# Optimization experiments

Hardware: AMD Instinct MI355X
Metric: run time of the kernel (lower is better)

The kernel has to match this reference:

```python
import jax, jax.numpy as jnp
import numpy as np

N = 20000      # nodes
E = 320000     # edges (before self loops)
F_IN = 256     # num_node_features
H = 8          # heads
C = 64         # dim_h per head
B = 64         # graphs in batch
NC = 10        # num_classes
HID = H * C    # 512


def setup_inputs() -> dict:
    key = jax.random.key(0)
    ks = jax.random.split(key, 20)
    def glorot(k, shape, fan):
        return jax.random.normal(k, shape, jnp.float32) / np.sqrt(fan)
    inp = {
        'x': jax.random.normal(ks[0], (N, F_IN), jnp.float32),
        'edge_index': jax.random.randint(ks[1], (2, E), 0, N),
        'batch': jnp.sort(jax.random.randint(ks[2], (N,), 0, B)),
        # conv1: F_IN -> H*C
        'W1': glorot(ks[3], (F_IN, HID), F_IN),
        'a_src1': glorot(ks[4], (H, C), C),
        'a_dst1': glorot(ks[5], (H, C), C),
        'b1': jnp.zeros((HID,), jnp.float32),
        # conv2: HID -> H*C
        'W2': glorot(ks[6], (HID, HID), HID),
        'a_src2': glorot(ks[7], (H, C), C),
        'a_dst2': glorot(ks[8], (H, C), C),
        'b2': jnp.zeros((HID,), jnp.float32),
        # conv3: HID -> H*C
        'W3': glorot(ks[9], (HID, HID), HID),
        'a_src3': glorot(ks[10], (H, C), C),
        'a_dst3': glorot(ks[11], (H, C), C),
        'b3': jnp.zeros((HID,), jnp.float32),
        # final classifier
        'Wl': glorot(ks[12], (HID, NC), HID),
        'bl': jnp.zeros((NC,), jnp.float32),
    }
    return inp


def _gat_conv(x, src, dst, W, a_src, a_dst, b):
    """PyG GATConv (concat=True, negative_slope=0.2). src/dst include self loops."""
    xt = (x @ W).reshape(-1, H, C)                      # [N, H, C]
    al_s = jnp.einsum('nhc,hc->nh', xt, a_src)          # [N, H]
    al_d = jnp.einsum('nhc,hc->nh', xt, a_dst)
    e = jax.nn.leaky_relu(al_s[src] + al_d[dst], 0.2)   # [E', H]
    m = jax.ops.segment_max(e, dst, num_segments=N)     # segment softmax (stable)
    m = jax.lax.stop_gradient(jnp.where(jnp.isfinite(m), m, 0.0))
    p = jnp.exp(e - m[dst])
    s = jax.ops.segment_sum(p, dst, num_segments=N)
    alpha = p / (s[dst] + 1e-16)                        # [E', H]
    msg = xt[src] * alpha[..., None]                    # [E', H, C]
    out = jax.ops.segment_sum(msg, dst, num_segments=N) # [N, H, C]
    return out.reshape(-1, HID) + b


def reference(x, edge_index, batch, W1, a_src1, a_dst1, b1,
              W2, a_src2, a_dst2, b2, W3, a_src3, a_dst3, b3, Wl, bl):
    loop = jnp.arange(N, dtype=edge_index.dtype)
    src = jnp.concatenate([edge_index[0], loop])        # add_self_loops=True
    dst = jnp.concatenate([edge_index[1], loop])

    h = jax.nn.elu(_gat_conv(x, src, dst, W1, a_src1, a_dst1, b1))
    h = jax.nn.elu(_gat_conv(h, src, dst, W2, a_src2, a_dst2, b2))
    h = jax.nn.elu(_gat_conv(h, src, dst, W3, a_src3, a_dst3, b3))

    # global mean pool over graphs
    cnt = jax.ops.segment_sum(jnp.ones((N,), h.dtype), batch, num_segments=B)
    hG = jax.ops.segment_sum(h, batch, num_segments=B) / jnp.clip(cnt, 1.0)[:, None]

    # dropout p=0.5 is identity in eval mode
    logits = hG @ Wl + bl
    return hG, jax.nn.softmax(logits, axis=1)
```

## Files before the change

kernel.cpp:

```cpp
#include <hip/hip_runtime.h>
#include <hip/hip_bf16.h>
#include <math.h>

#define N_NODES  20000
#define E_EDGES  320000
#define E_TOT    (E_EDGES + N_NODES)
#define F_INF    256
#define HEADS    8
#define CDIM     64
#define HID      512
#define B_GRAPHS 64
#define NCLS     10
#define M_PAD    20096
#define NSCAN    20
#define NWG_GEMM 1256

typedef __attribute__((ext_vector_type(8))) short short8;
typedef __attribute__((ext_vector_type(4))) float f32x4;

__device__ inline unsigned short f2bf(float x) {
    unsigned u = __builtin_bit_cast(unsigned, x);
    u += 0x7fff + ((u >> 16) & 1);
    return (unsigned short)(u >> 16);
}
__device__ inline float bf2f(unsigned short h) {
    unsigned u = ((unsigned)h) << 16;
    return __builtin_bit_cast(float, u);
}

#define GLOAD_LDS16(g, l) __builtin_amdgcn_global_load_lds(                     \
        (const __attribute__((address_space(1))) void*)(g),                     \
        (__attribute__((address_space(3))) void*)(l), 16, 0, 0)

__global__ __launch_bounds__(256) void split_pad(const float* __restrict__ src,
                                                 unsigned short* __restrict__ hi,
                                                 unsigned short* __restrict__ lo,
                                                 int M, int K, long total) {
    long i = ((long)blockIdx.x * 256 + threadIdx.x) * 4;
    if (i >= total) return;
    int row = (int)(i / K);
    float4 v = make_float4(0.f, 0.f, 0.f, 0.f);
    if (row < M) v = *(const float4*)(src + i);
    ushort4 h, l;
    h.x = f2bf(v.x); l.x = f2bf(v.x - bf2f(h.x));
    h.y = f2bf(v.y); l.y = f2bf(v.y - bf2f(h.y));
    h.z = f2bf(v.z); l.z = f2bf(v.z - bf2f(h.z));
    h.w = f2bf(v.w); l.w = f2bf(v.w - bf2f(h.w));
    *(ushort4*)(hi + i) = h;
    *(ushort4*)(lo + i) = l;
}

__global__ __launch_bounds__(256) void transpose_split_B(const float* __restrict__ B,
                                                         unsigned short* __restrict__ Bthi,
                                                         unsigned short* __restrict__ Btlo,
                                                         int K) {
    __shared__ float t[32][33];
    int n0 = blockIdx.x * 32, k0 = blockIdx.y * 32;
    int tx = threadIdx.x & 31, ty = threadIdx.x >> 5;
    for (int i = ty; i < 32; i += 8) t[i][tx] = B[(size_t)(k0 + i) * HID + n0 + tx];
    __syncthreads();
    for (int i = ty; i < 32; i += 8) {
        float v = t[tx][i];
        unsigned short h = f2bf(v);
        unsigned short l = f2bf(v - bf2f(h));
        Bthi[(size_t)(n0 + i) * K + k0 + tx] = h;
        Btlo[(size_t)(n0 + i) * K + k0 + tx] = l;
    }
}

__global__ __launch_bounds__(256) void gemm_mfma(const unsigned short* __restrict__ Ahi,
                                                 const unsigned short* __restrict__ Alo,
                                                 const unsigned short* __restrict__ Bhi,
                                                 const unsigned short* __restrict__ Blo,
                                                 const float* __restrict__ a_src,
                                                 const float* __restrict__ a_dst,
                                                 unsigned short* __restrict__ xtb,
                                                 float* __restrict__ al_s,
                                                 float* __restrict__ al_d,
                                                 int M, int K) {
    __shared__ short AsHi[4096], AsLo[4096], BsHi[2048], BsLo[2048];
    const int tid = threadIdx.x;
    const int w = tid >> 6, lane = tid & 63;

    const int xcd = blockIdx.x & 7, idx = blockIdx.x >> 3;
    const int wg = xcd * (NWG_GEMM >> 3) + idx;
    const int row0 = (wg >> 3) * 128, col0 = (wg & 7) * 64;

    long offA[2];
    int ldsA[2];
#pragma unroll
    for (int i = 0; i < 2; ++i) {
        int u = w * 128 + i * 64 + lane;
        int row = u >> 2;
        int kg = (u & 3) ^ ((row >> 1) & 3);
        offA[i] = ((long)(row0 + row) * K + kg * 8) * 2;
        ldsA[i] = (w * 128 + i * 64) * 8;
    }
    long offB;
    int ldsB;
    {
        int u = w * 64 + lane;
        int row = u >> 2;
        int kg = (u & 3) ^ ((row >> 1) & 3);
        offB = ((long)(col0 + row) * K + kg * 8) * 2;
        ldsB = (w * 64) * 8;
    }

    const int r16 = lane & 15, kg = lane >> 4;
    int aOff[2], bOff[4];
#pragma unroll
    for (int i = 0; i < 2; ++i) {
        int row = w * 32 + i * 16 + r16;
        aOff[i] = (row * 4 + (kg ^ ((row >> 1) & 3))) * 16;
    }
#pragma unroll
    for (int j = 0; j < 4; ++j) {
        int col = j * 16 + r16;
        bOff[j] = (col * 4 + (kg ^ ((col >> 1) & 3))) * 16;
    }

    const char* pAhi = (const char*)Ahi;
    const char* pAlo = (const char*)Alo;
    const char* pBhi = (const char*)Bhi;
    const char* pBlo = (const char*)Blo;

    f32x4 acc[2][4] = {};

    for (int kk = 0; kk < K; kk += 32) {
        long kb = (long)kk * 2;
        __syncthreads();
#pragma unroll
        for (int i = 0; i < 2; ++i) {
            GLOAD_LDS16(pAhi + offA[i] + kb, AsHi + ldsA[i]);
            GLOAD_LDS16(pAlo + offA[i] + kb, AsLo + ldsA[i]);
        }
        GLOAD_LDS16(pBhi + offB + kb, BsHi + ldsB);
        GLOAD_LDS16(pBlo + offB + kb, BsLo + ldsB);
        __syncthreads();

        short8 fah[2], fal[2], fbh[4], fbl[4];
#pragma unroll
        for (int i = 0; i < 2; ++i) {
            fah[i] = *(const short8*)((const char*)AsHi + aOff[i]);
            fal[i] = *(const short8*)((const char*)AsLo + aOff[i]);
        }
#pragma unroll
        for (int j = 0; j < 4; ++j) {
            fbh[j] = *(const short8*)((const char*)BsHi + bOff[j]);
            fbl[j] = *(const short8*)((const char*)BsLo + bOff[j]);
        }
#pragma unroll
        for (int i = 0; i < 2; ++i)
#pragma unroll
            for (int j = 0; j < 4; ++j) {
                acc[i][j] = __builtin_amdgcn_mfma_f32_16x16x32_bf16(fah[i], fbh[j], acc[i][j], 0, 0, 0);
                acc[i][j] = __builtin_amdgcn_mfma_f32_16x16x32_bf16(fah[i], fbl[j], acc[i][j], 0, 0, 0);
                acc[i][j] = __builtin_amdgcn_mfma_f32_16x16x32_bf16(fal[i], fbh[j], acc[i][j], 0, 0, 0);
            }
    }

    const int h = col0 >> 6;
    float asv[4], adv[4];
#pragma unroll
    for (int j = 0; j < 4; ++j) {
        asv[j] = a_src[h * CDIM + j * 16 + r16];
        adv[j] = a_dst[h * CDIM + j * 16 + r16];
    }
#pragma unroll
    for (int i = 0; i < 2; ++i) {
        int rbase = row0 + w * 32 + i * 16 + (lane >> 4) * 4;
#pragma unroll
        for (int rr = 0; rr < 4; ++rr) {
            float ss = acc[i][0][rr] * asv[0] + acc[i][1][rr] * asv[1]
                     + acc[i][2][rr] * asv[2] + acc[i][3][rr] * asv[3];
            float dd = acc[i][0][rr] * adv[0] + acc[i][1][rr] * adv[1]
                     + acc[i][2][rr] * adv[2] + acc[i][3][rr] * adv[3];
#pragma unroll
            for (int off = 1; off < 16; off <<= 1) {
                ss += __shfl_xor(ss, off);
                dd += __shfl_xor(dd, off);
            }
            int row = rbase + rr;
            if ((lane & 15) == 0 && row < M) {
                al_s[row * HEADS + h] = ss;
                al_d[row * HEADS + h] = dd;
            }
        }
#pragma unroll
        for (int j = 0; j < 4; ++j) {
            int col = col0 + j * 16 + r16;
#pragma unroll
            for (int rr = 0; rr < 4; ++rr)
                if (rbase + rr < M) xtb[(size_t)(rbase + rr) * HID + col] = f2bf(acc[i][j][rr]);
        }
    }
}

__global__ __launch_bounds__(256) void count_edges(const int* __restrict__ ei,
                                                   int* __restrict__ counts) {
    int e = blockIdx.x * 256 + threadIdx.x;
    if (e < E_TOT) {
        int dst = (e < E_EDGES) ? ei[E_EDGES + e] : (e - E_EDGES);
        atomicAdd(&counts[dst], 1);
    }
}

__global__ __launch_bounds__(1024) void scan_local(const int* __restrict__ counts,
                                                   int* __restrict__ incl,
                                                   int* __restrict__ bsum,
                                                   const int* __restrict__ batch,
                                                   int* __restrict__ bounds) {
    __shared__ int s[1024];
    int tid = threadIdx.x;
    int i = blockIdx.x * 1024 + tid;
    if (blockIdx.x == 0 && tid <= B_GRAPHS) {
        int lo = 0, hi = N_NODES;
        while (lo < hi) {
            int mid = (lo + hi) >> 1;
            if (batch[mid] < tid) lo = mid + 1; else hi = mid;
        }
        bounds[tid] = lo;
    }
    int v = (i < N_NODES) ? counts[i] : 0;
    s[tid] = v;
    __syncthreads();
    for (int off = 1; off < 1024; off <<= 1) {
        int t = (tid >= off) ? s[tid - off] : 0;
        __syncthreads();
        s[tid] += t;
        __syncthreads();
    }
    if (i < N_NODES) incl[i] = s[tid];
    if (tid == 1023) bsum[blockIdx.x] = s[1023];
}

__global__ __launch_bounds__(1024) void scan_finalize(const int* __restrict__ counts,
                                                      const int* __restrict__ incl,
                                                      const int* __restrict__ bsum,
                                                      int* __restrict__ offsets,
                                                      int* __restrict__ cursor) {
    __shared__ int bpre_s;
    if (threadIdx.x == 0) {
        int s = 0;
        for (int j = 0; j < blockIdx.x; ++j) s += bsum[j];
        bpre_s = s;
    }
    __syncthreads();
    int i = blockIdx.x * 1024 + threadIdx.x;
    if (i < N_NODES) {
        int inc = incl[i] + bpre_s;
        offsets[i + 1] = inc;
        cursor[i] = inc - counts[i];
    }
    if (i == 0) offsets[0] = 0;
}

__global__ __launch_bounds__(256) void scatter_edges(const int* __restrict__ ei,
                                                     int* __restrict__ cursor,
                                                     int* __restrict__ csr) {
    int e = blockIdx.x * 256 + threadIdx.x;
    if (e < E_TOT) {
        int srcn, dst;
        if (e < E_EDGES) { srcn = ei[e]; dst = ei[E_EDGES + e]; }
        else             { srcn = dst = e - E_EDGES; }
        int pos = atomicAdd(&cursor[dst], 1);
        csr[pos] = srcn;
    }
}

__global__ __launch_bounds__(256) void gat_aggregate4(const unsigned short* __restrict__ xtb,
                                                      const float* __restrict__ al_s,
                                                      const float* __restrict__ al_d,
                                                      const int* __restrict__ offsets,
                                                      const int* __restrict__ csr,
                                                      const float* __restrict__ bias,
                                                      unsigned short* __restrict__ outHi,
                                                      unsigned short* __restrict__ outLo) {
    const int lane = threadIdx.x & 63;
    const int n = blockIdx.x * 4 + (threadIdx.x >> 6);
    const int h = lane >> 3;
    const int c0 = lane * 8;
    const int beg = offsets[n];
    const int deg = offsets[n + 1] - beg;
    const float aldv = al_d[n * HEADS + h];

    float acc[8] = {};
    float psum = 0.f;

#pragma unroll 4
    for (int i = 0; i < deg; ++i) {
        int srcn = csr[beg + i];
        float ev = al_s[srcn * HEADS + h] + aldv;
        ev = (ev >= 0.f) ? ev : 0.2f * ev;
        float p = __expf(ev);
        psum += p;
        short8 row = *(const short8*)(xtb + (size_t)srcn * HID + c0);
#pragma unroll
        for (int j = 0; j < 8; ++j)
            acc[j] = fmaf(p, bf2f((unsigned short)row[j]), acc[j]);
    }

    const float inv = 1.f / (psum + 1e-16f);
    float4 b0 = *(const float4*)(bias + c0);
    float4 b1 = *(const float4*)(bias + c0 + 4);
    float bv[8] = { b0.x, b0.y, b0.z, b0.w, b1.x, b1.y, b1.z, b1.w };
    short8 h8, l8;
#pragma unroll
    for (int j = 0; j < 8; ++j) {
        float v = acc[j] * inv + bv[j];
        v = (v > 0.f) ? v : expm1f(v);
        unsigned short hi = f2bf(v);
        h8[j] = (short)hi;
        l8[j] = (short)f2bf(v - bf2f(hi));
    }
    size_t o = (size_t)n * HID + c0;
    *(short8*)(outHi + o) = h8;
    *(short8*)(outLo + o) = l8;
}

__global__ __launch_bounds__(256) void pool_partial(const unsigned short* __restrict__ hHi,
                                                    const unsigned short* __restrict__ hLo,
                                                    const int* __restrict__ bounds,
                                                    float* __restrict__ partial) {
    const int b = blockIdx.x, y = blockIdx.y, k = blockIdx.z;
    const int s = bounds[b], cnt = bounds[b + 1] - s;
    const int ns = s + (cnt * k) / 4;
    const int ne = s + (cnt * (k + 1)) / 4;
    const int t = threadIdx.x;
    const int chp = t & 31;
    const int nl = t >> 5;

    float a0 = 0.f, a1 = 0.f;
    for (int n = ns + nl; n < ne; n += 8) {
        size_t off = (size_t)n * HID + y * 64 + chp * 2;
        unsigned vh = *(const unsigned*)(hHi + off);
        unsigned vl = *(const unsigned*)(hLo + off);
        a0 += bf2f((unsigned short)(vh & 0xffff)) + bf2f((unsigned short)(vl & 0xffff));
        a1 += bf2f((unsigned short)(vh >> 16)) + bf2f((unsigned short)(vl >> 16));
    }
    __shared__ float red[4][32][2];
    a0 += __shfl_xor(a0, 32);
    a1 += __shfl_xor(a1, 32);
    if ((t & 63) < 32) { red[t >> 6][chp][0] = a0; red[t >> 6][chp][1] = a1; }
    __syncthreads();
    if (t < 64) {
        int cp = t >> 1, c = t & 1;
        float v = red[0][cp][c] + red[1][cp][c] + red[2][cp][c] + red[3][cp][c];
        partial[(((size_t)k * B_GRAPHS + b) * 8 + y) * 64 + cp * 2 + c] = v;
    }
}

__global__ __launch_bounds__(512) void pool_classify(const float* __restrict__ partial,
                                                     const int* __restrict__ bounds,
                                                     const float* __restrict__ Wl,
                                                     const float* __restrict__ bl,
                                                     float* __restrict__ hG,
                                                     float* __restrict__ outP) {
    const int b = blockIdx.x, t = threadIdx.x;
    __shared__ float row[HID];
    __shared__ float logit[NCLS];
    float v = 0.f;
#pragma unroll
    for (int k = 0; k < 4; ++k)
        v += partial[((size_t)k * B_GRAPHS + b) * HID + t];
    float cnt = fmaxf((float)(bounds[b + 1] - bounds[b]), 1.0f);
    v /= cnt;
    hG[b * HID + t] = v;
    row[t] = v;
    __syncthreads();
    if (t < NCLS) {
        float acc = bl[t];
        for (int j = 0; j < HID; ++j) acc += row[j] * Wl[j * NCLS + t];
        logit[t] = acc;
    }
    __syncthreads();
    if (t == 0) {
        float mx = logit[0];
        for (int k = 1; k < NCLS; ++k) mx = fmaxf(mx, logit[k]);
        float ssum = 0.f, ex[NCLS];
        for (int k = 0; k < NCLS; ++k) { ex[k] = expf(logit[k] - mx); ssum += ex[k]; }
        for (int k = 0; k < NCLS; ++k) outP[b * NCLS + k] = ex[k] / ssum;
    }
}

extern "C" void kernel_launch(void* const* d_in, const int* in_sizes, int n_in,
                              void* d_out, int out_size, void* d_ws, size_t ws_size,
                              hipStream_t stream) {
    const float* x     = (const float*)d_in[0];
    const int*   ei    = (const int*)d_in[1];
    const int*   batch = (const int*)d_in[2];
    const float* W[3]  = { (const float*)d_in[3], (const float*)d_in[7],  (const float*)d_in[11] };
    const float* as_[3] = { (const float*)d_in[4], (const float*)d_in[8],  (const float*)d_in[12] };
    const float* ad_[3] = { (const float*)d_in[5], (const float*)d_in[9],  (const float*)d_in[13] };
    const float* bb[3] = { (const float*)d_in[6], (const float*)d_in[10], (const float*)d_in[14] };
    const float* Wl    = (const float*)d_in[15];
    const float* bl    = (const float*)d_in[16];

    char* ws = (char*)d_ws;
    unsigned short* A1hi = (unsigned short*)ws;      ws += (size_t)M_PAD * F_INF * 2;
    unsigned short* A1lo = (unsigned short*)ws;      ws += (size_t)M_PAD * F_INF * 2;
    unsigned short* A2hi = (unsigned short*)ws;      ws += (size_t)M_PAD * HID * 2;
    unsigned short* A2lo = (unsigned short*)ws;      ws += (size_t)M_PAD * HID * 2;
    unsigned short* Bthi = (unsigned short*)ws;      ws += (size_t)HID * HID * 2;
    unsigned short* Btlo = (unsigned short*)ws;      ws += (size_t)HID * HID * 2;
    unsigned short* xtb  = (unsigned short*)ws;      ws += (size_t)N_NODES * HID * 2;
    float* als  = (float*)ws;                        ws += (size_t)N_NODES * HEADS * 4;
    float* ald  = (float*)ws;                        ws += (size_t)N_NODES * HEADS * 4;
    float* partial = (float*)ws;                     ws += (size_t)4 * B_GRAPHS * HID * 4;
    int* counts  = (int*)ws;                         ws += (size_t)N_NODES * 4;
    int* incl    = (int*)ws;                         ws += (size_t)N_NODES * 4;
    int* bsum    = (int*)ws;                         ws += 32 * 4;
    int* offsets = (int*)ws;                         ws += (size_t)(N_NODES + 1) * 4;
    int* cursor  = (int*)ws;                         ws += (size_t)N_NODES * 4;
    int* csr     = (int*)ws;                         ws += (size_t)E_TOT * 4;
    int* bounds  = (int*)ws;                         ws += (size_t)(B_GRAPHS + 1) * 4;

    float* hG = (float*)d_out;
    float* probs = (float*)d_out + (size_t)B_GRAPHS * HID;

    hipMemsetAsync(counts, 0, (size_t)N_NODES * 4, stream);
    count_edges<<<(E_TOT + 255) / 256, 256, 0, stream>>>(ei, counts);
    scan_local<<<NSCAN, 1024, 0, stream>>>(counts, incl, bsum, batch, bounds);
    scan_finalize<<<NSCAN, 1024, 0, stream>>>(counts, incl, bsum, offsets, cursor);
    scatter_edges<<<(E_TOT + 255) / 256, 256, 0, stream>>>(ei, cursor, csr);
    hipMemsetAsync(A2hi + (size_t)N_NODES * HID, 0, (size_t)(M_PAD - N_NODES) * HID * 2, stream);
    hipMemsetAsync(A2lo + (size_t)N_NODES * HID, 0, (size_t)(M_PAD - N_NODES) * HID * 2, stream);

    {
        long totA = (long)M_PAD * F_INF;
        split_pad<<<(int)(totA / 4 / 256), 256, 0, stream>>>(x, A1hi, A1lo, N_NODES, F_INF, totA);
        transpose_split_B<<<dim3(HID / 32, F_INF / 32), 256, 0, stream>>>(W[0], Bthi, Btlo, F_INF);
        gemm_mfma<<<NWG_GEMM, 256, 0, stream>>>(A1hi, A1lo, Bthi, Btlo, as_[0], ad_[0],
                                                xtb, als, ald, N_NODES, F_INF);
        gat_aggregate4<<<N_NODES / 4, 256, 0, stream>>>(xtb, als, ald, offsets, csr, bb[0], A2hi, A2lo);
    }

    for (int L = 1; L < 3; ++L) {
        transpose_split_B<<<dim3(HID / 32, HID / 32), 256, 0, stream>>>(W[L], Bthi, Btlo, HID);
        gemm_mfma<<<NWG_GEMM, 256, 0, stream>>>(A2hi, A2lo, Bthi, Btlo, as_[L], ad_[L],
                                                xtb, als, ald, N_NODES, HID);
        gat_aggregate4<<<N_NODES / 4, 256, 0, stream>>>(xtb, als, ald, offsets, csr, bb[L], A2hi, A2lo);
    }

    {
        dim3 pgrid(B_GRAPHS, 8, 4);
        pool_partial<<<pgrid, 256, 0, stream>>>(A2hi, A2lo, bounds, partial);
        pool_classify<<<B_GRAPHS, 512, 0, stream>>>(partial, bounds, Wl, bl, hG, probs);
    }
}
```

Measured before the change: 379.4 us.

## Double-buffer GEMM LDS tiles and batch all weight transposes into one launch

The GEMM main loop now uses two LDS buffers, issuing the async global-to-LDS loads for the next K-slice before computing the current one, with explicit vmcnt waits and raw barriers in place of two __syncthreads per iteration. The three per-layer weight transpose/split kernels are merged into a single 3D-grid launch at the start, writing into separate per-layer buffers. This aims to hide global-load latency behind MFMA work and remove two kernel launches. The cost is doubled LDS use per workgroup, which may reduce occupancy, plus extra workspace for the weight copies.

```diff
diff --git a/kernel.cpp b/kernel.cpp
--- a/kernel.cpp
+++ b/kernel.cpp
@@ -50,10 +50,22 @@
     *(ushort4*)(lo + i) = l;
 }
 
-__global__ __launch_bounds__(256) void transpose_split_B(const float* __restrict__ B,
-                                                         unsigned short* __restrict__ Bthi,
-                                                         unsigned short* __restrict__ Btlo,
-                                                         int K) {
+__global__ __launch_bounds__(256) void transpose_split_all(const float* __restrict__ W1,
+                                                           const float* __restrict__ W2,
+                                                           const float* __restrict__ W3,
+                                                           unsigned short* __restrict__ B1h,
+                                                           unsigned short* __restrict__ B1l,
+                                                           unsigned short* __restrict__ B2h,
+                                                           unsigned short* __restrict__ B2l,
+                                                           unsigned short* __restrict__ B3h,
+                                                           unsigned short* __restrict__ B3l) {
+    const int L = blockIdx.z;
+    const int K = (L == 0) ? F_INF : HID;
+    if (blockIdx.y * 32 >= K) return;
+    const float* B = (L == 0) ? W1 : (L == 1) ? W2 : W3;
+    unsigned short* Bh = (L == 0) ? B1h : (L == 1) ? B2h : B3h;
+    unsigned short* Bl = (L == 0) ? B1l : (L == 1) ? B2l : B3l;
+
     __shared__ float t[32][33];
     int n0 = blockIdx.x * 32, k0 = blockIdx.y * 32;
     int tx = threadIdx.x & 31, ty = threadIdx.x >> 5;
@@ -63,8 +75,8 @@
         float v = t[tx][i];
         unsigned short h = f2bf(v);
         unsigned short l = f2bf(v - bf2f(h));
-        Bthi[(size_t)(n0 + i) * K + k0 + tx] = h;
-        Btlo[(size_t)(n0 + i) * K + k0 + tx] = l;
+        Bh[(size_t)(n0 + i) * K + k0 + tx] = h;
+        Bl[(size_t)(n0 + i) * K + k0 + tx] = l;
     }
 }
 
@@ -78,7 +90,7 @@
                                                  float* __restrict__ al_s,
                                                  float* __restrict__ al_d,
                                                  int M, int K) {
-    __shared__ short AsHi[4096], AsLo[4096], BsHi[2048], BsLo[2048];
+    __shared__ short AsHi[2][4096], AsLo[2][4096], BsHi[2][2048], BsLo[2][2048];
     const int tid = threadIdx.x;
     const int w = tid >> 6, lane = tid & 63;
 
@@ -126,38 +138,57 @@
 
     f32x4 acc[2][4] = {};
 
-    for (int kk = 0; kk < K; kk += 32) {
-        long kb = (long)kk * 2;
-        __syncthreads();
-#pragma unroll
-        for (int i = 0; i < 2; ++i) {
-            GLOAD_LDS16(pAhi + offA[i] + kb, AsHi + ldsA[i]);
-            GLOAD_LDS16(pAlo + offA[i] + kb, AsLo + ldsA[i]);
+#define STAGE(buf, kk) do {                                                      \
+        long kb = (long)(kk) * 64;                                               \
+        _Pragma("unroll")                                                        \
+        for (int i_ = 0; i_ < 2; ++i_) {                                         \
+            GLOAD_LDS16(pAhi + offA[i_] + kb, &AsHi[buf][ldsA[i_]]);             \
+            GLOAD_LDS16(pAlo + offA[i_] + kb, &AsLo[buf][ldsA[i_]]);             \
+        }                                                                        \
+        GLOAD_LDS16(pBhi + offB + kb, &BsHi[buf][ldsB]);                         \
+        GLOAD_LDS16(pBlo + offB + kb, &BsLo[buf][ldsB]);                         \
+    } while (0)
+
+#define COMPUTE(buf) do {                                                        \
+        short8 fah[2], fal[2], fbh[4], fbl[4];                                   \
+        _Pragma("unroll")                                                        \
+        for (int i_ = 0; i_ < 2; ++i_) {                                         \
+            fah[i_] = *(const short8*)((const char*)AsHi[buf] + aOff[i_]);       \
+            fal[i_] = *(const short8*)((const char*)AsLo[buf] + aOff[i_]);       \
+        }                                                                        \
+        _Pragma("unroll")                                                        \
+        for (int j_ = 0; j_ < 4; ++j_) {                                         \
+            fbh[j_] = *(const short8*)((const char*)BsHi[buf] + bOff[j_]);       \
+            fbl[j_] = *(const short8*)((const char*)BsLo[buf] + bOff[j_]);       \
+        }                                                                        \
+        _Pragma("unroll")                                                        \
+        for (int i_ = 0; i_ < 2; ++i_)                                           \
+            _Pragma("unroll")                                                    \
+            for (int j_ = 0; j_ < 4; ++j_) {                                     \
+                acc[i_][j_] = __builtin_amdgcn_mfma_f32_16x16x32_bf16(fah[i_], fbh[j_], acc[i_][j_], 0, 0, 0); \
+                acc[i_][j_] = __builtin_amdgcn_mfma_f32_16x16x32_bf16(fah[i_], fbl[j_], acc[i_][j_], 0, 0, 0); \
+                acc[i_][j_] = __builtin_amdgcn_mfma_f32_16x16x32_bf16(fal[i_], fbh[j_], acc[i_][j_], 0, 0, 0); \
+            }                                                                    \
+    } while (0)
+
+    const int NS = K >> 5;
+    STAGE(0, 0);
+    int cur = 0;
+    for (int t = 0; t < NS; ++t) {
+        if (t + 1 < NS) {
+            STAGE(cur ^ 1, t + 1);
+            asm volatile("s_waitcnt vmcnt(6)" ::: "memory");
+        } else {
+            asm volatile("s_waitcnt vmcnt(0)" ::: "memory");
         }
-        GLOAD_LDS16(pBhi + offB + kb, BsHi + ldsB);
-        GLOAD_LDS16(pBlo + offB + kb, BsLo + ldsB);
-        __syncthreads();
-
-        short8 fah[2], fal[2], fbh[4], fbl[4];
-#pragma unroll
-        for (int i = 0; i < 2; ++i) {
-            fah[i] = *(const short8*)((const char*)AsHi + aOff[i]);
-            fal[i] = *(const short8*)((const char*)AsLo + aOff[i]);
-        }
-#pragma unroll
-        for (int j = 0; j < 4; ++j) {
-            fbh[j] = *(const short8*)((const char*)BsHi + bOff[j]);
-            fbl[j] = *(const short8*)((const char*)BsLo + bOff[j]);
-        }
-#pragma unroll
-        for (int i = 0; i < 2; ++i)
-#pragma unroll
-            for (int j = 0; j < 4; ++j) {
-                acc[i][j] = __builtin_amdgcn_mfma_f32_16x16x32_bf16(fah[i], fbh[j], acc[i][j], 0, 0, 0);
-                acc[i][j] = __builtin_amdgcn_mfma_f32_16x16x32_bf16(fah[i], fbl[j], acc[i][j], 0, 0, 0);
-                acc[i][j] = __builtin_amdgcn_mfma_f32_16x16x32_bf16(fal[i], fbh[j], acc[i][j], 0, 0, 0);
-            }
-    }
+        __builtin_amdgcn_s_barrier();
+        COMPUTE(cur);
+        __builtin_amdgcn_s_barrier();
+        cur ^= 1;
+    }
+
+#undef STAGE
+#undef COMPUTE
 
     const int h = col0 >> 6;
     float asv[4], adv[4];
@@ -401,8 +432,12 @@
     unsigned short* A1lo = (unsigned short*)ws;      ws += (size_t)M_PAD * F_INF * 2;
     unsigned short* A2hi = (unsigned short*)ws;      ws += (size_t)M_PAD * HID * 2;
     unsigned short* A2lo = (unsigned short*)ws;      ws += (size_t)M_PAD * HID * 2;
-    unsigned short* Bthi = (unsigned short*)ws;      ws += (size_t)HID * HID * 2;
-    unsigned short* Btlo = (unsigned short*)ws;      ws += (size_t)HID * HID * 2;
+    unsigned short* Bt1h = (unsigned short*)ws;      ws += (size_t)HID * F_INF * 2;
+    unsigned short* Bt1l = (unsigned short*)ws;      ws += (size_t)HID * F_INF * 2;
+    unsigned short* Bt2h = (unsigned short*)ws;      ws += (size_t)HID * HID * 2;
+    unsigned short* Bt2l = (unsigned short*)ws;      ws += (size_t)HID * HID * 2;
+    unsigned short* Bt3h = (unsigned short*)ws;      ws += (size_t)HID * HID * 2;
+    unsigned short* Bt3l = (unsigned short*)ws;      ws += (size_t)HID * HID * 2;
     unsigned short* xtb  = (unsigned short*)ws;      ws += (size_t)N_NODES * HID * 2;
     float* als  = (float*)ws;                        ws += (size_t)N_NODES * HEADS * 4;
     float* ald  = (float*)ws;                        ws += (size_t)N_NODES * HEADS * 4;
@@ -419,28 +454,30 @@
     float* probs = (float*)d_out + (size_t)B_GRAPHS * HID;
 
     hipMemsetAsync(counts, 0, (size_t)N_NODES * 4, stream);
+    transpose_split_all<<<dim3(16, 16, 3), 256, 0, stream>>>(W[0], W[1], W[2],
+                                                             Bt1h, Bt1l, Bt2h, Bt2l, Bt3h, Bt3l);
     count_edges<<<(E_TOT + 255) / 256, 256, 0, stream>>>(ei, counts);
     scan_local<<<NSCAN, 1024, 0, stream>>>(counts, incl, bsum, batch, bounds);
     scan_finalize<<<NSCAN, 1024, 0, stream>>>(counts, incl, bsum, offsets, cursor);
     scatter_edges<<<(E_TOT + 255) / 256, 256, 0, stream>>>(ei, cursor, csr);
     hipMemsetAsync(A2hi + (size_t)N_NODES * HID, 0, (size_t)(M_PAD - N_NODES) * HID * 2, stream);
     hipMemsetAsync(A2lo + (size_t)N_NODES * HID, 0, (size_t)(M_PAD - N_NODES) * HID * 2, stream);
-
     {
         long totA = (long)M_PAD * F_INF;
         split_pad<<<(int)(totA / 4 / 256), 256, 0, stream>>>(x, A1hi, A1lo, N_NODES, F_INF, totA);
-        transpose_split_B<<<dim3(HID / 32, F_INF / 32), 256, 0, stream>>>(W[0], Bthi, Btlo, F_INF);
-        gemm_mfma<<<NWG_GEMM, 256, 0, stream>>>(A1hi, A1lo, Bthi, Btlo, as_[0], ad_[0],
-                                                xtb, als, ald, N_NODES, F_INF);
-        gat_aggregate4<<<N_NODES / 4, 256, 0, stream>>>(xtb, als, ald, offsets, csr, bb[0], A2hi, A2lo);
-    }
-
-    for (int L = 1; L < 3; ++L) {
-        transpose_split_B<<<dim3(HID / 32, HID / 32), 256, 0, stream>>>(W[L], Bthi, Btlo, HID);
-        gemm_mfma<<<NWG_GEMM, 256, 0, stream>>>(A2hi, A2lo, Bthi, Btlo, as_[L], ad_[L],
-                                                xtb, als, ald, N_NODES, HID);
-        gat_aggregate4<<<N_NODES / 4, 256, 0, stream>>>(xtb, als, ald, offsets, csr, bb[L], A2hi, A2lo);
-    }
+    }
+
+    gemm_mfma<<<NWG_GEMM, 256, 0, stream>>>(A1hi, A1lo, Bt1h, Bt1l, as_[0], ad_[0],
+                                            xtb, als, ald, N_NODES, F_INF);
+    gat_aggregate4<<<N_NODES / 4, 256, 0, stream>>>(xtb, als, ald, offsets, csr, bb[0], A2hi, A2lo);
+
+    gemm_mfma<<<NWG_GEMM, 256, 0, stream>>>(A2hi, A2lo, Bt2h, Bt2l, as_[1], ad_[1],
+                                            xtb, als, ald, N_NODES, HID);
+    gat_aggregate4<<<N_NODES / 4, 256, 0, stream>>>(xtb, als, ald, offsets, csr, bb[1], A2hi, A2lo);
+
+    gemm_mfma<<<NWG_GEMM, 256, 0, stream>>>(A2hi, A2lo, Bt3h, Bt3l, as_[2], ad_[2],
+                                            xtb, als, ald, N_NODES, HID);
+    gat_aggregate4<<<N_NODES / 4, 256, 0, stream>>>(xtb, als, ald, offsets, csr, bb[2], A2hi, A2lo);
 
     {
         dim3 pgrid(B_GRAPHS, 8, 4);
```

Measured after the change: 368.5 us, median of 2. -2.9%, faster.
